# Kernel optimization log

Measured on AMD Instinct MI355X. Metric: run time of the kernel, lower is better.

The kernel has to match this reference:

```python
import jax, jax.numpy as jnp
import numpy as np

STRIDE = 1
PAD = 1
KH = KW = 3


def _conv2d(x, w, b, stride, pad):
    out = jax.lax.conv_general_dilated(
        x, w, window_strides=(stride, stride),
        padding=[(pad, pad), (pad, pad)],
        dimension_numbers=("NCHW", "OIHW", "NCHW"))
    return out + b[None, :, None, None]


def _deform_conv2d(x, offset, mask, weight, stride, pad):
    """Modulated deformable conv v2 (torchvision deform_conv2d semantics, no bias).

    x: [B,C,H,W]  offset: [B,2*K2,Ho,Wo] (dy,dx interleaved per tap)
    mask: [B,K2,Ho,Wo]  weight: [O,C,KH,KW]
    """
    B, C, H, W = x.shape
    O = weight.shape[0]
    K2 = KH * KW
    Ho, Wo = offset.shape[2], offset.shape[3]

    dy = offset[:, 0::2]  # [B,K2,Ho,Wo]
    dx = offset[:, 1::2]

    # base sampling grid per kernel tap k = i*KW + j
    ki = jnp.repeat(jnp.arange(KH), KW)  # [K2]
    kj = jnp.tile(jnp.arange(KW), KH)    # [K2]
    base_y = (jnp.arange(Ho) * stride - pad)[None, :, None] + ki[:, None, None]  # [K2,Ho,1]
    base_x = (jnp.arange(Wo) * stride - pad)[None, None, :] + kj[:, None, None]  # [K2,1,Wo]

    py = base_y[None].astype(x.dtype) + dy  # [B,K2,Ho,Wo]
    px = base_x[None].astype(x.dtype) + dx

    y0f = jnp.floor(py)
    x0f = jnp.floor(px)
    wy = py - y0f  # bilinear weights
    wx = px - x0f
    y0 = y0f.astype(jnp.int32)
    x0 = x0f.astype(jnp.int32)

    x_flat = x.reshape(B, C, H * W)

    def gather(yi, xi):
        # zero padding: out-of-range integer neighbors contribute 0
        valid = (yi >= 0) & (yi < H) & (xi >= 0) & (xi < W)
        idx = jnp.clip(yi, 0, H - 1) * W + jnp.clip(xi, 0, W - 1)  # [B,K2,Ho,Wo]
        g = jax.vmap(lambda xf, id_: xf[:, id_])(x_flat, idx)      # [B,C,K2,Ho,Wo]
        return g * valid[:, None].astype(x.dtype)

    v00 = gather(y0, x0)
    v01 = gather(y0, x0 + 1)
    v10 = gather(y0 + 1, x0)
    v11 = gather(y0 + 1, x0 + 1)

    wy_ = wy[:, None]  # [B,1,K2,Ho,Wo]
    wx_ = wx[:, None]
    val = (v00 * (1 - wy_) * (1 - wx_) + v01 * (1 - wy_) * wx_
           + v10 * wy_ * (1 - wx_) + v11 * wy_ * wx_)
    val = val * mask[:, None]

    # conv accumulation over (C, K2)
    return jnp.einsum("bckhw,ock->bohw", val, weight.reshape(O, C, K2))


def setup_inputs() -> dict:
    key = jax.random.key(0)
    ks = jax.random.split(key, 6)
    B, C, O, H, W = 4, 128, 128, 64, 64
    x = jax.random.normal(ks[0], (B, C, H, W), dtype=jnp.float32)
    org_w = jax.random.normal(ks[1], (O, C, KH, KW), dtype=jnp.float32) * 0.05
    offset_w = jax.random.normal(ks[2], (2 * KH * KW, C, 3, 3), dtype=jnp.float32) * 0.01
    offset_b = jax.random.normal(ks[3], (2 * KH * KW,), dtype=jnp.float32) * 0.01
    mask_w = jax.random.normal(ks[4], (KH * KW, C, 3, 3), dtype=jnp.float32) * 0.01
    mask_b = jax.random.normal(ks[5], (KH * KW,), dtype=jnp.float32) * 0.01
    return {"x": x, "org_w": org_w, "offset_w": offset_w, "offset_b": offset_b,
            "mask_w": mask_w, "mask_b": mask_b}


def reference(x, org_w, offset_w, offset_b, mask_w, mask_b):
    offset = _conv2d(x, offset_w, offset_b, STRIDE, 1)          # [B,18,H,W]
    mask = jax.nn.sigmoid(_conv2d(x, mask_w, mask_b, STRIDE, 1))  # [B,9,H,W]
    return _deform_conv2d(x, offset, mask, org_w, STRIDE, PAD)
```

## Files before the change

### kernel.cpp

```cpp
#include <hip/hip_runtime.h>
#include <hip/hip_bf16.h>
#include <cmath>

#define B_    4
#define C_    128
#define O_    128
#define K2T   9
#define CK    1152
#define NPIX  4096
#define ROWS  8
#define BUFC  512
#define BUFF  8192
#define NGRP  36

using bf16   = __bf16;
using bf16x4 = __attribute__((ext_vector_type(4))) __bf16;
using bf16x8 = __attribute__((ext_vector_type(8))) __bf16;
using f32x4  = __attribute__((ext_vector_type(4))) float;

#define WS_WBF 0
#define WS_WOM 294912

__global__ void __launch_bounds__(256) repack_kernel(
    const float* __restrict__ org_w, const float* __restrict__ offset_w,
    const float* __restrict__ mask_w, bf16* __restrict__ w_bf,
    bf16* __restrict__ wom_bf) {
  int t = blockIdx.x * 256 + threadIdx.x;
  if (t >= 160 * CK) return;
  int row = t / CK, r = t % CK;
  int cc = r / 288, rr = r % 288;
  int k = rr >> 5, cq = rr & 31;
  int c = cc * 32 + cq;
  if (row < 128) {
    w_bf[t] = (bf16)org_w[((size_t)row * C_ + c) * K2T + k];
  } else {
    int ch = row - 128;
    float v = 0.f;
    if (ch < 18)      v = offset_w[((size_t)ch * C_ + c) * K2T + k];
    else if (ch < 27) v = mask_w[((size_t)(ch - 18) * C_ + c) * K2T + k];
    wom_bf[(size_t)ch * CK + r] = (bf16)v;
  }
}

__device__ __forceinline__ void gl_lds16(const float* src, float* lds_uniform) {
  __builtin_amdgcn_global_load_lds(
      (const __attribute__((address_space(1))) void*)src,
      (__attribute__((address_space(3))) void*)lds_uniform, 16, 0, 0);
}

__global__ void __launch_bounds__(576) deform_fused_kernel(
    const float* __restrict__ x, const bf16* __restrict__ w_bf,
    const bf16* __restrict__ wom_bf, const float* __restrict__ off_b,
    const float* __restrict__ mask_b, float* __restrict__ out) {
  __shared__ __align__(16) float xslab[3 * BUFF];
  __shared__ __align__(16) bf16  valbuf[NGRP * 512];
  __shared__ __align__(16) float S_lds[32 * 64];

  int tid  = threadIdx.x;
  int bid0 = blockIdx.x;
  int bid  = (bid0 & 7) * 32 + (bid0 >> 3);
  int b    = bid >> 6, ho = bid & 63;
  int lane = tid & 63, wv = tid >> 6;
  int l15  = lane & 15, l4 = lane >> 4;
  bool w8  = (wv < 8);

  const float* xb = x + (size_t)b * C_ * NPIX;
  float* xs3 = xslab;

  f32x4 acc1 = {};
  {
    int mf  = wv & 1, nfq = wv >> 1;
    const bf16* wbase1 = wom_bf + (size_t)(mf * 16 + l15) * CK + l4 * 8;
    const bf16* vb1    = valbuf + l4 * 512 + (nfq * 16 + l15) * 8;
    int p  = lane;
    int g2 = wv;
    for (int cc = 0; cc < 4; ++cc) {
      __syncthreads();
#pragma unroll
      for (int i = 0; i < 3; ++i) {
        int slot = tid + i * 576;
        if (slot < 1536) {
          int ch = slot / 48, rem2 = slot % 48;
          int row = rem2 / 16, c16 = rem2 & 15;
          int y = ho - 1 + row;
          float4 v = make_float4(0.f, 0.f, 0.f, 0.f);
          if ((unsigned)y < 64u)
            v = *((const float4*)(xb + (size_t)(cc * 32 + ch) * NPIX + y * 64) + c16);
          *(float4*)(&xs3[ch * 192 + row * 64 + c16 * 4]) = v;
        }
      }
      __syncthreads();
      if (g2 < 8) {
#pragma unroll
        for (int k = 0; k < 9; ++k) {
          int ki = k / 3, kj = k % 3;
          int px = p - 1 + kj;
          bf16x4 pr;
#pragma unroll
          for (int cqi = 0; cqi < 4; ++cqi) {
            int cq = (g2 << 2) + cqi;
            float v = ((unsigned)px < 64u) ? xs3[cq * 192 + ki * 64 + px] : 0.f;
            pr[cqi] = (bf16)v;
          }
          *(bf16x4*)(valbuf + (k * 4 + (g2 >> 1)) * 512 + p * 8 + (g2 & 1) * 4) = pr;
        }
      }
      __syncthreads();
      if (w8) {
        __builtin_amdgcn_s_setprio(1);
#pragma unroll
        for (int ks = 0; ks < 9; ++ks) {
          bf16x8 a  = *(const bf16x8*)(wbase1 + cc * 288 + ks * 32);
          bf16x8 bv = *(const bf16x8*)(vb1 + ks * 2048);
          acc1 = __builtin_amdgcn_mfma_f32_16x16x32_bf16(a, bv, acc1, 0, 0, 0);
        }
        __builtin_amdgcn_s_setprio(0);
      }
    }
  }
  __syncthreads();
  if (w8) {
    int mf = wv & 1, nfq = wv >> 1;
    int so = mf * 16 + l4 * 4;
    int sp = nfq * 16 + l15;
#pragma unroll
    for (int r = 0; r < 4; ++r) S_lds[(so + r) * 64 + sp] = acc1[r];
  }
  __syncthreads();

  auto stage = [&](int it2) {
    if (w8 && it2 < 8) {
      int ccs = it2 >> 1, g2s = it2 & 1;
      float* dstb = xslab + (it2 % 3) * BUFF;
#pragma unroll
      for (int u = 0; u < 2; ++u) {
        int chl = 2 * wv + u;
        int ch  = ccs * 32 + g2s * 16 + chl;
        const float* srcb = xb + (size_t)ch * NPIX + l15 * 4;
        float* dst = dstb + chl * BUFC;
#pragma unroll
        for (int j = 0; j < 2; ++j) {
          int y = ho - 3 + j * 4 + l4;
          y = y < 0 ? 0 : (y > 63 ? 63 : y);
          gl_lds16(srcb + y * 64, dst + j * 256);
        }
      }
    }
  };

  stage(0);
  stage(1);
  __builtin_amdgcn_sched_barrier(0);

  float pw0, pw1, pw2, pw3;
  int   psa, psb, vg;
  {
    int k = wv, p = lane;
    float dy = S_lds[(2 * k) * 64 + p]     + off_b[2 * k];
    float dx = S_lds[(2 * k + 1) * 64 + p] + off_b[2 * k + 1];
    float mz = S_lds[(18 + k) * 64 + p]    + mask_b[k];
    float m  = 1.f / (1.f + expf(-mz));
    int ki = k / 3, kj = k % 3;
    float py = (float)(ho - 1 + ki) + dy;
    float px = (float)(p  - 1 + kj) + dx;
    float fy = floorf(py), fx = floorf(px);
    int y0 = (int)fy, x0 = (int)fx;
    float wy = py - fy, wx = px - fx;
    float vy0 = ((unsigned)y0       < 64u) ? 1.f : 0.f;
    float vy1 = ((unsigned)(y0 + 1) < 64u) ? 1.f : 0.f;
    float vx0 = ((unsigned)x0       < 64u) ? 1.f : 0.f;
    float vx1 = ((unsigned)(x0 + 1) < 64u) ? 1.f : 0.f;
    int r0  = y0 - (ho - 3);
    int ir0 = r0 < 0 ? 0 : (r0 > ROWS - 2 ? ROWS - 2 : r0);
    int c0  = x0 < 0 ? 0 : (x0 > 63 ? 63 : x0);
    int x1  = x0 + 1;
    int c1  = x1 < 0 ? 0 : (x1 > 63 ? 63 : x1);
    pw0 = (1.f - wy) * (1.f - wx) * m * vy0 * vx0;
    pw1 = (1.f - wy) * wx         * m * vy0 * vx1;
    pw2 = wy * (1.f - wx)         * m * vy1 * vx0;
    pw3 = wy * wx                 * m * vy1 * vx1;
    psa = ir0 * 64 + c0;
    psb = ir0 * 64 + c1;
    vg  = k * 4;
  }

  f32x4 acc[4] = {};
  bf16x8 aF[9] = {};
  const bf16* wbase = w_bf + (size_t)(wv * 16 + l15) * CK + l4 * 8;
  const bf16* vbase = valbuf + l4 * 512 + l15 * 8;

  auto sample = [&](const float* sbuf, int g2s) {
#pragma unroll
    for (int h = 0; h < 2; ++h) {
      bf16x8 pack;
#pragma unroll
      for (int j = 0; j < 8; ++j) {
        const float* cb = sbuf + (h * 8 + j) * BUFC;
        float a0 = cb[psa], a1 = cb[psa + 64];
        float b0 = cb[psb], b1 = cb[psb + 64];
        pack[j] = (bf16)(pw0 * a0 + pw1 * b0 + pw2 * a1 + pw3 * b1);
      }
      *(bf16x8*)(valbuf + (vg + g2s * 2 + h) * 512 + lane * 8) = pack;
    }
  };

#pragma unroll 1
  for (int cc = 0; cc < 4; ++cc) {
    int it0 = 2 * cc;
    asm volatile("s_waitcnt vmcnt(4)" ::: "memory");
    __builtin_amdgcn_s_barrier();
    __builtin_amdgcn_sched_barrier(0);
    if (w8) {
#pragma unroll
      for (int ks = 0; ks < 9; ++ks)
        aF[ks] = *(const bf16x8*)(wbase + cc * 288 + ks * 32);
    }
    __builtin_amdgcn_sched_barrier(0);
    stage(it0 + 2);
    __builtin_amdgcn_sched_barrier(0);
    sample(xslab + (it0 % 3) * BUFF, 0);
    if (cc < 3) asm volatile("s_waitcnt vmcnt(4)" ::: "memory");
    else        asm volatile("s_waitcnt vmcnt(0)" ::: "memory");
    __builtin_amdgcn_s_barrier();
    __builtin_amdgcn_sched_barrier(0);
    stage(it0 + 3);
    __builtin_amdgcn_sched_barrier(0);
    sample(xslab + ((it0 + 1) % 3) * BUFF, 1);
    asm volatile("s_waitcnt lgkmcnt(0)" ::: "memory");
    __builtin_amdgcn_s_barrier();
    __builtin_amdgcn_sched_barrier(0);
    if (w8) {
      __builtin_amdgcn_s_setprio(1);
#pragma unroll
      for (int ks = 0; ks < 9; ++ks) {
#pragma unroll
        for (int nf = 0; nf < 4; ++nf) {
          bf16x8 bv = *(const bf16x8*)(vbase + ks * 2048 + nf * 128);
          acc[nf] = __builtin_amdgcn_mfma_f32_16x16x32_bf16(aF[ks], bv, acc[nf], 0, 0, 0);
        }
      }
      __builtin_amdgcn_s_setprio(0);
    }
  }

  if (w8) {
    float* ob = out + (size_t)b * O_ * NPIX + ho * 64;
#pragma unroll
    for (int nf = 0; nf < 4; ++nf)
#pragma unroll
      for (int r = 0; r < 4; ++r) {
        int o = wv * 16 + l4 * 4 + r;
        int p = nf * 16 + l15;
        ob[(size_t)o * NPIX + p] = acc[nf][r];
      }
  }
}

extern "C" void kernel_launch(void* const* d_in, const int* in_sizes, int n_in,
                              void* d_out, int out_size, void* d_ws, size_t ws_size,
                              hipStream_t stream) {
  const float* x        = (const float*)d_in[0];
  const float* org_w    = (const float*)d_in[1];
  const float* offset_w = (const float*)d_in[2];
  const float* off_b    = (const float*)d_in[3];
  const float* mask_w   = (const float*)d_in[4];
  const float* mask_b   = (const float*)d_in[5];
  float* out = (float*)d_out;
  char*  ws  = (char*)d_ws;

  bf16* w_bf   = (bf16*)(ws + WS_WBF);
  bf16* wom_bf = (bf16*)(ws + WS_WOM);

  repack_kernel<<<720, 256, 0, stream>>>(org_w, offset_w, mask_w, w_bf, wom_bf);
  deform_fused_kernel<<<256, 576, 0, stream>>>(x, w_bf, wom_bf, off_b, mask_b, out);
}
```

Baseline: 47.48 us.

## Fold offset/mask conv into the shared async-staged 16-step pipeline

The offset/mask 3x3 conv previously ran as a separate phase. It used synchronous global-to-register-to-LDS loads and extra syncthreads before the deformable pass. Now both passes share one 16-half-step loop that streams x slabs through the triple-buffered async LDS pipeline, using a fixed im2col gather for the first eight steps and bilinear sampling after. This removes the serial, latency-exposed prologue, but x is loaded twice through the async path and the loop body gains branching and register pressure.

Measured after the change: 45.93 us. -3.3%, faster.

```diff
diff --git a/kernel.cpp b/kernel.cpp
--- a/kernel.cpp
+++ b/kernel.cpp
@@ -14,7 +14,6 @@
 #define NGRP  36
 
 using bf16   = __bf16;
-using bf16x4 = __attribute__((ext_vector_type(4))) __bf16;
 using bf16x8 = __attribute__((ext_vector_type(8))) __bf16;
 using f32x4  = __attribute__((ext_vector_type(4))) float;
 
@@ -65,72 +64,10 @@
   bool w8  = (wv < 8);
 
   const float* xb = x + (size_t)b * C_ * NPIX;
-  float* xs3 = xslab;
-
-  f32x4 acc1 = {};
-  {
-    int mf  = wv & 1, nfq = wv >> 1;
-    const bf16* wbase1 = wom_bf + (size_t)(mf * 16 + l15) * CK + l4 * 8;
-    const bf16* vb1    = valbuf + l4 * 512 + (nfq * 16 + l15) * 8;
-    int p  = lane;
-    int g2 = wv;
-    for (int cc = 0; cc < 4; ++cc) {
-      __syncthreads();
-#pragma unroll
-      for (int i = 0; i < 3; ++i) {
-        int slot = tid + i * 576;
-        if (slot < 1536) {
-          int ch = slot / 48, rem2 = slot % 48;
-          int row = rem2 / 16, c16 = rem2 & 15;
-          int y = ho - 1 + row;
-          float4 v = make_float4(0.f, 0.f, 0.f, 0.f);
-          if ((unsigned)y < 64u)
-            v = *((const float4*)(xb + (size_t)(cc * 32 + ch) * NPIX + y * 64) + c16);
-          *(float4*)(&xs3[ch * 192 + row * 64 + c16 * 4]) = v;
-        }
-      }
-      __syncthreads();
-      if (g2 < 8) {
-#pragma unroll
-        for (int k = 0; k < 9; ++k) {
-          int ki = k / 3, kj = k % 3;
-          int px = p - 1 + kj;
-          bf16x4 pr;
-#pragma unroll
-          for (int cqi = 0; cqi < 4; ++cqi) {
-            int cq = (g2 << 2) + cqi;
-            float v = ((unsigned)px < 64u) ? xs3[cq * 192 + ki * 64 + px] : 0.f;
-            pr[cqi] = (bf16)v;
-          }
-          *(bf16x4*)(valbuf + (k * 4 + (g2 >> 1)) * 512 + p * 8 + (g2 & 1) * 4) = pr;
-        }
-      }
-      __syncthreads();
-      if (w8) {
-        __builtin_amdgcn_s_setprio(1);
-#pragma unroll
-        for (int ks = 0; ks < 9; ++ks) {
-          bf16x8 a  = *(const bf16x8*)(wbase1 + cc * 288 + ks * 32);
-          bf16x8 bv = *(const bf16x8*)(vb1 + ks * 2048);
-          acc1 = __builtin_amdgcn_mfma_f32_16x16x32_bf16(a, bv, acc1, 0, 0, 0);
-        }
-        __builtin_amdgcn_s_setprio(0);
-      }
-    }
-  }
-  __syncthreads();
-  if (w8) {
-    int mf = wv & 1, nfq = wv >> 1;
-    int so = mf * 16 + l4 * 4;
-    int sp = nfq * 16 + l15;
-#pragma unroll
-    for (int r = 0; r < 4; ++r) S_lds[(so + r) * 64 + sp] = acc1[r];
-  }
-  __syncthreads();
 
   auto stage = [&](int it2) {
-    if (w8 && it2 < 8) {
-      int ccs = it2 >> 1, g2s = it2 & 1;
+    if (w8 && it2 < 16) {
+      int ccs = (it2 & 7) >> 1, g2s = it2 & 1;
       float* dstb = xslab + (it2 % 3) * BUFF;
 #pragma unroll
       for (int u = 0; u < 2; ++u) {
@@ -148,98 +85,139 @@
     }
   };
 
+  float apw; int apsa;
+  {
+    int k = wv, p = lane;
+    int ki = k / 3, kj = k % 3;
+    int row = ho - 1 + ki, colu = p - 1 + kj;
+    bool ok = ((unsigned)row < 64u) && ((unsigned)colu < 64u);
+    int cc0 = colu < 0 ? 0 : (colu > 63 ? 63 : colu);
+    apw  = ok ? 1.f : 0.f;
+    apsa = (ki + 2) * 64 + cc0;
+  }
+
   stage(0);
   stage(1);
   __builtin_amdgcn_sched_barrier(0);
 
-  float pw0, pw1, pw2, pw3;
-  int   psa, psb, vg;
-  {
-    int k = wv, p = lane;
-    float dy = S_lds[(2 * k) * 64 + p]     + off_b[2 * k];
-    float dx = S_lds[(2 * k + 1) * 64 + p] + off_b[2 * k + 1];
-    float mz = S_lds[(18 + k) * 64 + p]    + mask_b[k];
-    float m  = 1.f / (1.f + expf(-mz));
-    int ki = k / 3, kj = k % 3;
-    float py = (float)(ho - 1 + ki) + dy;
-    float px = (float)(p  - 1 + kj) + dx;
-    float fy = floorf(py), fx = floorf(px);
-    int y0 = (int)fy, x0 = (int)fx;
-    float wy = py - fy, wx = px - fx;
-    float vy0 = ((unsigned)y0       < 64u) ? 1.f : 0.f;
-    float vy1 = ((unsigned)(y0 + 1) < 64u) ? 1.f : 0.f;
-    float vx0 = ((unsigned)x0       < 64u) ? 1.f : 0.f;
-    float vx1 = ((unsigned)(x0 + 1) < 64u) ? 1.f : 0.f;
-    int r0  = y0 - (ho - 3);
-    int ir0 = r0 < 0 ? 0 : (r0 > ROWS - 2 ? ROWS - 2 : r0);
-    int c0  = x0 < 0 ? 0 : (x0 > 63 ? 63 : x0);
-    int x1  = x0 + 1;
-    int c1  = x1 < 0 ? 0 : (x1 > 63 ? 63 : x1);
-    pw0 = (1.f - wy) * (1.f - wx) * m * vy0 * vx0;
-    pw1 = (1.f - wy) * wx         * m * vy0 * vx1;
-    pw2 = wy * (1.f - wx)         * m * vy1 * vx0;
-    pw3 = wy * wx                 * m * vy1 * vx1;
-    psa = ir0 * 64 + c0;
-    psb = ir0 * 64 + c1;
-    vg  = k * 4;
-  }
-
+  f32x4 acc1 = {};
   f32x4 acc[4] = {};
-  bf16x8 aF[9] = {};
-  const bf16* wbase = w_bf + (size_t)(wv * 16 + l15) * CK + l4 * 8;
-  const bf16* vbase = valbuf + l4 * 512 + l15 * 8;
-
-  auto sample = [&](const float* sbuf, int g2s) {
-#pragma unroll
-    for (int h = 0; h < 2; ++h) {
-      bf16x8 pack;
-#pragma unroll
-      for (int j = 0; j < 8; ++j) {
-        const float* cb = sbuf + (h * 8 + j) * BUFC;
-        float a0 = cb[psa], a1 = cb[psa + 64];
-        float b0 = cb[psb], b1 = cb[psb + 64];
-        pack[j] = (bf16)(pw0 * a0 + pw1 * b0 + pw2 * a1 + pw3 * b1);
-      }
-      *(bf16x8*)(valbuf + (vg + g2s * 2 + h) * 512 + lane * 8) = pack;
-    }
-  };
+  bf16x8 aF[9];
+  float pw0 = 0.f, pw1 = 0.f, pw2 = 0.f, pw3 = 0.f;
+  int   psa = 0, psb = 0;
+  int   mf = wv & 1, nfq = wv >> 1;
+  const bf16* wbase1 = wom_bf + (size_t)(mf * 16 + l15) * CK + l4 * 8;
+  const bf16* wbase  = w_bf  + (size_t)(wv * 16 + l15) * CK + l4 * 8;
+  const bf16* vb1    = valbuf + l4 * 512 + (nfq * 16 + l15) * 8;
+  const bf16* vbase  = valbuf + l4 * 512 + l15 * 8;
 
 #pragma unroll 1
-  for (int cc = 0; cc < 4; ++cc) {
-    int it0 = 2 * cc;
-    asm volatile("s_waitcnt vmcnt(4)" ::: "memory");
+  for (int hp = 0; hp < 16; ++hp) {
+    int c2 = hp >> 1;
+    bool passB = (c2 >= 4);
+    int cc = c2 & 3;
+    if (hp == 15) asm volatile("s_waitcnt vmcnt(0)" ::: "memory");
+    else          asm volatile("s_waitcnt vmcnt(4)" ::: "memory");
     __builtin_amdgcn_s_barrier();
     __builtin_amdgcn_sched_barrier(0);
-    if (w8) {
-#pragma unroll
-      for (int ks = 0; ks < 9; ++ks)
-        aF[ks] = *(const bf16x8*)(wbase + cc * 288 + ks * 32);
-    }
+    if (!(hp & 1) && w8) {
+      const bf16* ab = (passB ? wbase : wbase1) + cc * 288;
+#pragma unroll
+      for (int ks = 0; ks < 9; ++ks) aF[ks] = *(const bf16x8*)(ab + ks * 32);
+      __builtin_amdgcn_sched_barrier(0);
+    }
+    stage(hp + 2);
     __builtin_amdgcn_sched_barrier(0);
-    stage(it0 + 2);
-    __builtin_amdgcn_sched_barrier(0);
-    sample(xslab + (it0 % 3) * BUFF, 0);
-    if (cc < 3) asm volatile("s_waitcnt vmcnt(4)" ::: "memory");
-    else        asm volatile("s_waitcnt vmcnt(0)" ::: "memory");
-    __builtin_amdgcn_s_barrier();
-    __builtin_amdgcn_sched_barrier(0);
-    stage(it0 + 3);
-    __builtin_amdgcn_sched_barrier(0);
-    sample(xslab + ((it0 + 1) % 3) * BUFF, 1);
-    asm volatile("s_waitcnt lgkmcnt(0)" ::: "memory");
-    __builtin_amdgcn_s_barrier();
-    __builtin_amdgcn_sched_barrier(0);
-    if (w8) {
-      __builtin_amdgcn_s_setprio(1);
-#pragma unroll
-      for (int ks = 0; ks < 9; ++ks) {
-#pragma unroll
-        for (int nf = 0; nf < 4; ++nf) {
-          bf16x8 bv = *(const bf16x8*)(vbase + ks * 2048 + nf * 128);
-          acc[nf] = __builtin_amdgcn_mfma_f32_16x16x32_bf16(aF[ks], bv, acc[nf], 0, 0, 0);
-        }
-      }
-      __builtin_amdgcn_s_setprio(0);
+    {
+      const float* sbuf = xslab + (hp % 3) * BUFF;
+      int grp = wv * 4 + (hp & 1) * 2;
+      if (passB) {
+#pragma unroll
+        for (int h = 0; h < 2; ++h) {
+          bf16x8 pack;
+#pragma unroll
+          for (int j = 0; j < 8; ++j) {
+            const float* cb = sbuf + (h * 8 + j) * BUFC;
+            float a0 = cb[psa], a1 = cb[psa + 64];
+            float b0 = cb[psb], b1 = cb[psb + 64];
+            pack[j] = (bf16)(pw0 * a0 + pw1 * b0 + pw2 * a1 + pw3 * b1);
+          }
+          *(bf16x8*)(valbuf + (grp + h) * 512 + lane * 8) = pack;
+        }
+      } else {
+#pragma unroll
+        for (int h = 0; h < 2; ++h) {
+          bf16x8 pack;
+#pragma unroll
+          for (int j = 0; j < 8; ++j)
+            pack[j] = (bf16)(apw * sbuf[(h * 8 + j) * BUFC + apsa]);
+          *(bf16x8*)(valbuf + (grp + h) * 512 + lane * 8) = pack;
+        }
+      }
+    }
+    if (hp & 1) {
+      asm volatile("s_waitcnt lgkmcnt(0)" ::: "memory");
+      __builtin_amdgcn_s_barrier();
+      __builtin_amdgcn_sched_barrier(0);
+      if (w8) {
+        __builtin_amdgcn_s_setprio(1);
+        if (passB) {
+#pragma unroll
+          for (int ks = 0; ks < 9; ++ks) {
+#pragma unroll
+            for (int nf = 0; nf < 4; ++nf) {
+              bf16x8 bv = *(const bf16x8*)(vbase + ks * 2048 + nf * 128);
+              acc[nf] = __builtin_amdgcn_mfma_f32_16x16x32_bf16(aF[ks], bv, acc[nf], 0, 0, 0);
+            }
+          }
+        } else {
+#pragma unroll
+          for (int ks = 0; ks < 9; ++ks) {
+            bf16x8 bv = *(const bf16x8*)(vb1 + ks * 2048);
+            acc1 = __builtin_amdgcn_mfma_f32_16x16x32_bf16(aF[ks], bv, acc1, 0, 0, 0);
+          }
+        }
+        __builtin_amdgcn_s_setprio(0);
+      }
+    }
+    if (hp == 7) {
+      if (w8) {
+        int so = mf * 16 + l4 * 4;
+        int sp = nfq * 16 + l15;
+#pragma unroll
+        for (int r = 0; r < 4; ++r) S_lds[(so + r) * 64 + sp] = acc1[r];
+      }
+      asm volatile("s_waitcnt lgkmcnt(0)" ::: "memory");
+      __builtin_amdgcn_s_barrier();
+      __builtin_amdgcn_sched_barrier(0);
+      {
+        int k = wv, p = lane;
+        float dy = S_lds[(2 * k) * 64 + p]     + off_b[2 * k];
+        float dx = S_lds[(2 * k + 1) * 64 + p] + off_b[2 * k + 1];
+        float mz = S_lds[(18 + k) * 64 + p]    + mask_b[k];
+        float m  = 1.f / (1.f + expf(-mz));
+        int ki = k / 3, kj = k % 3;
+        float py = (float)(ho - 1 + ki) + dy;
+        float px = (float)(p  - 1 + kj) + dx;
+        float fy = floorf(py), fx = floorf(px);
+        int y0 = (int)fy, x0 = (int)fx;
+        float wy = py - fy, wx = px - fx;
+        float vy0 = ((unsigned)y0       < 64u) ? 1.f : 0.f;
+        float vy1 = ((unsigned)(y0 + 1) < 64u) ? 1.f : 0.f;
+        float vx0 = ((unsigned)x0       < 64u) ? 1.f : 0.f;
+        float vx1 = ((unsigned)(x0 + 1) < 64u) ? 1.f : 0.f;
+        int r0  = y0 - (ho - 3);
+        int ir0 = r0 < 0 ? 0 : (r0 > ROWS - 2 ? ROWS - 2 : r0);
+        int c0  = x0 < 0 ? 0 : (x0 > 63 ? 63 : x0);
+        int x1  = x0 + 1;
+        int c1  = x1 < 0 ? 0 : (x1 > 63 ? 63 : x1);
+        pw0 = (1.f - wy) * (1.f - wx) * m * vy0 * vx0;
+        pw1 = (1.f - wy) * wx         * m * vy0 * vx1;
+        pw2 = wy * (1.f - wx)         * m * vy1 * vx0;
+        pw3 = wy * wx                 * m * vy1 * vx1;
+        psa = ir0 * 64 + c0;
+        psb = ir0 * 64 + c1;
+      }
     }
   }
 
```
